# Kernel tuning notes

Measured on AMD Instinct MI355X. Metric: run time of the kernel, lower is better.

Reference implementation:

```python
import jax, jax.numpy as jnp
import numpy as np

B, T, N, DIN = 32, 12, 512, 1
H, K, ED, HOR, OD = 64, 3, 10, 12, 1


def setup_inputs() -> dict:
    key = jax.random.key(0)
    ks = jax.random.split(key, 15)
    rn = lambda k, s, sc=0.1: jax.random.normal(k, s, jnp.float32) * sc
    return {
        "source": jax.random.normal(ks[0], (B, T, N, DIN), jnp.float32),
        "targets": jax.random.normal(ks[1], (B, HOR, N, OD), jnp.float32),
        # standard Gumbel(0,1) noise: -log(Exp(1)), matches torch's exponential_().log()
        "gumbel_noise": -jnp.log(jax.random.exponential(ks[2], (N, N, 2), jnp.float32)),
        "emb": jax.random.normal(ks[3], (N, ED), jnp.float32),
        "gw0": rn(ks[4], (ED, K, DIN + H, 2 * H)),
        "gb0": rn(ks[5], (ED, 2 * H)),
        "uw0": rn(ks[6], (ED, K, DIN + H, H)),
        "ub0": rn(ks[7], (ED, H)),
        "gw1": rn(ks[8], (ED, K, 2 * H, 2 * H)),
        "gb1": rn(ks[9], (ED, 2 * H)),
        "uw1": rn(ks[10], (ED, K, 2 * H, H)),
        "ub1": rn(ks[11], (ED, H)),
        "cw": rn(ks[12], (HOR * OD, 1, 1, H)),  # Conv2d(1, HOR*OD, (1, H)) weight
        "cb": rn(ks[13], (HOR * OD,)),
    }


def scaled_laplacian(emb, gnoise):
    sim = emb @ emb.T                                   # [N,N]
    nrm = jnp.linalg.norm(emb, axis=1, keepdims=True)
    lg = sim / (nrm @ nrm.T)
    lg = (lg + 1.0) / 2.0
    logits = jnp.stack([lg, 1.0 - lg], axis=-1)         # [N,N,2]
    # faithful to the pasted gumbel_softmax: y_soft = gumbels (no softmax), tau=1, hard=True
    y_soft = logits + gnoise
    idx = jnp.argmax(y_soft, axis=-1)
    y_hard = jax.nn.one_hot(idx, 2, dtype=logits.dtype)
    ret = y_hard - jax.lax.stop_gradient(y_soft) + y_soft
    adj = ret[:, :, 0] * (1.0 - jnp.eye(N, dtype=logits.dtype))  # zero diagonal
    d = jnp.sum(adj, axis=1)
    L = -adj + jnp.diag(d)                              # diag(adj)=0, so L diag = d
    lam = jnp.max(L) - jnp.min(L)
    tilde = 2.0 * L / lam - jnp.eye(N, dtype=logits.dtype)
    return tilde


def cheb_supports(tilde):
    sup = [jnp.eye(N, dtype=tilde.dtype), tilde]
    for _ in range(2, K):
        sup.append(2.0 * tilde @ sup[-1] - sup[-2])
    return jnp.stack(sup, axis=0)                       # [K,N,N]


def gconv(x, emb, supports, wp, bp):
    # x: [B,N,C]; wp: [ED,K,C,O]; bp: [ED,O]
    xg = jnp.einsum('knm,bmc->bnkc', supports, x)
    w = jnp.einsum('nd,dkio->nkio', emb, wp)
    b = emb @ bp                                        # [N,O]
    return jnp.einsum('bnki,nkio->bno', xg, w) + b


def run_layer(inputs, emb, supports, gw, gb, uw, ub):
    # inputs: [B,T,N,C] -> hidden states [B,T,N,H]
    h0 = jnp.zeros((inputs.shape[0], N, H), inputs.dtype)

    def step(h, x_t):
        xs = jnp.concatenate([x_t, h], axis=-1)
        zr = jax.nn.sigmoid(gconv(xs, emb, supports, gw, gb))
        z, r = zr[..., :H], zr[..., H:]
        cand = jnp.concatenate([x_t, z * h], axis=-1)
        hc = jnp.tanh(gconv(cand, emb, supports, uw, ub))
        h_new = r * h + (1.0 - r) * hc
        return h_new, h_new

    _, hs = jax.lax.scan(step, h0, jnp.swapaxes(inputs, 0, 1))
    return jnp.swapaxes(hs, 0, 1)


def reference(source, targets, gumbel_noise, emb, gw0, gb0, uw0, ub0,
              gw1, gb1, uw1, ub1, cw, cb):
    tilde = scaled_laplacian(emb, gumbel_noise)
    supports = cheb_supports(tilde)
    h1 = run_layer(source, emb, supports, gw0, gb0, uw0, ub0)
    h2 = run_layer(h1, emb, supports, gw1, gb1, uw1, ub1)
    last = h2[:, -1, :, :]                              # [B,N,H]
    # Conv2d(1, HOR*OD, (1,H)) over [B,1,N,H] == per-node linear
    y = jnp.einsum('bnh,oh->bon', last, cw[:, 0, 0, :]) + cb[None, :, None]
    y = y.reshape(-1, HOR, OD, N)
    return jnp.transpose(y, (0, 1, 3, 2))               # [B,HOR,N,OD]
```

## Files before the change

kernel.cpp:

```cpp
#include <hip/hip_runtime.h>
#include <math.h>

#define N_    512
#define B_    32
#define T_    12
#define H_    64
#define ED_   10
#define HOR_  12
#define OUTS_ 4096

typedef unsigned short ushort_t;
typedef __attribute__((ext_vector_type(4))) float f32x4;
typedef __attribute__((ext_vector_type(8))) __bf16 bf16x8;
typedef __attribute__((ext_vector_type(8))) short short8;

__device__ __forceinline__ float sigmoidf_(float x){ return 1.f/(1.f+expf(-x)); }
__device__ __forceinline__ float b2f(ushort_t u){ return __uint_as_float(((unsigned)u)<<16); }
__device__ __forceinline__ ushort_t f2b(float f){
  unsigned x = __float_as_uint(f);
  unsigned r = x + 0x7FFFu + ((x>>16)&1u);
  return (ushort_t)(r>>16);
}
__device__ __forceinline__ void stage16(const void* g, void* l){
  __builtin_amdgcn_global_load_lds(
    (const __attribute__((address_space(1))) unsigned int*)g,
    (__attribute__((address_space(3))) unsigned int*)l, 16, 0, 0);
}

__global__ __launch_bounds__(512) void k_norm(const float* __restrict__ emb, float* __restrict__ nrm){
  int n = threadIdx.x;
  if (n < N_){
    float s = 0.f;
    #pragma unroll
    for (int d=0; d<ED_; ++d){ float v = emb[n*ED_+d]; s += v*v; }
    nrm[n] = sqrtf(s);
  }
}

__global__ __launch_bounds__(256) void k_adj(const float* __restrict__ emb, const float* __restrict__ nrm,
                      const float* __restrict__ gn, ushort_t* __restrict__ Abf, float* __restrict__ dvec){
  __shared__ float ei[ED_];
  __shared__ float red[256];
  int i = blockIdx.x;
  if (threadIdx.x < ED_) ei[threadIdx.x] = emb[i*ED_+threadIdx.x];
  __syncthreads();
  float ni = nrm[i];
  float part = 0.f;
  for (int j = threadIdx.x; j < N_; j += 256){
    float dot = 0.f;
    #pragma unroll
    for (int d=0; d<ED_; ++d) dot += ei[d]*emb[j*ED_+d];
    float lg = (dot/(ni*nrm[j]) + 1.f)*0.5f;
    size_t gi = ((size_t)i*N_ + j)*2;
    float y0 = lg + gn[gi];
    float y1 = (1.f - lg) + gn[gi+1];
    bool a = (j != i && y0 >= y1);
    Abf[(size_t)i*N_ + j] = a ? (ushort_t)0x3F80 : (ushort_t)0;
    part += a ? 1.f : 0.f;
  }
  red[threadIdx.x] = part;
  __syncthreads();
  for (int s=128; s>0; s>>=1){
    if (threadIdx.x < s) red[threadIdx.x] += red[threadIdx.x+s];
    __syncthreads();
  }
  if (threadIdx.x==0) dvec[i] = red[0];
}

__global__ __launch_bounds__(512) void k_lam(const float* __restrict__ dvec, float* __restrict__ lam){
  __shared__ float red[512];
  red[threadIdx.x] = dvec[threadIdx.x];
  __syncthreads();
  for (int s=256; s>0; s>>=1){
    if (threadIdx.x < s) red[threadIdx.x] = fmaxf(red[threadIdx.x], red[threadIdx.x+s]);
    __syncthreads();
  }
  if (threadIdx.x==0){
    float maxd = red[0];
    lam[0] = maxd + (maxd > 0.f ? 1.f : 0.f);
  }
}

__global__ __launch_bounds__(256) void k_a2(const ushort_t* __restrict__ Abf, ushort_t* __restrict__ A2bf){
  __shared__ float ar[N_];
  int n = blockIdx.x;
  for (int p = threadIdx.x; p < N_; p += 256) ar[p] = b2f(Abf[(size_t)n*N_ + p]);
  __syncthreads();
  int m0 = threadIdx.x, m1 = threadIdx.x + 256;
  float a0 = 0.f, a1 = 0.f;
  for (int p=0; p<N_; ++p){
    float ap = ar[p];
    a0 += ap * b2f(Abf[(size_t)p*N_ + m0]);
    a1 += ap * b2f(Abf[(size_t)p*N_ + m1]);
  }
  A2bf[(size_t)n*N_ + m0] = f2b(a0);
  A2bf[(size_t)n*N_ + m1] = f2b(a1);
}

__global__ __launch_bounds__(256) void k_admats(const ushort_t* __restrict__ Abf, const float* __restrict__ dvec,
                        const float* __restrict__ lam, ushort_t* __restrict__ ADh){
  int idx = blockIdx.x*256 + threadIdx.x;
  int m = idx & (N_-1);
  float dm = 2.f*dvec[m]/lam[0] - 1.f;
  ADh[idx] = Abf[idx] ? f2b(dm) : (ushort_t)0;
}

__global__ __launch_bounds__(256) void k_apply(
    const ushort_t* __restrict__ XH, const ushort_t* __restrict__ XL,
    const ushort_t* __restrict__ Abf, const ushort_t* __restrict__ A2bf, const ushort_t* __restrict__ ADh,
    float* __restrict__ P, float* __restrict__ Rm, float* __restrict__ Qm)
{
  __shared__ ushort_t lds[5*4096];
  const int cBase = blockIdx.x<<6, nBase = blockIdx.y<<6;
  const int tid = threadIdx.x, lane = tid&63, w = tid>>6;
  const int lrow = lane>>3, lslot = lane&7;
  const int srck = lslot ^ (lrow&7);
  f32x4 acc[3][4];
  #pragma unroll
  for (int i=0;i<3;++i)
    #pragma unroll
    for (int j=0;j<4;++j) acc[i][j] = f32x4{0.f,0.f,0.f,0.f};
  const int fl = lane&15, kq = lane>>4;

  for (int kk=0; kk<512; kk+=64){
    #pragma unroll
    for (int s=0; s<10; ++s){
      int instId = w + s*4;
      int tile = instId>>3;
      int inst = instId&7;
      const char* g = (tile==0)? (const char*)XH : (tile==1)? (const char*)XL :
                      (tile==2)? (const char*)Abf : (tile==3)? (const char*)A2bf : (const char*)ADh;
      int rb = (tile<2? cBase : nBase) + inst*8 + lrow;
      stage16(g + (size_t)rb*(N_*2) + kk*2 + srck*16,
              (char*)lds + tile*8192 + inst*1024);
    }
    __syncthreads();
    #pragma unroll
    for (int kh=0; kh<2; ++kh){
      int rowA = (w<<4) + fl;
      int offA = (rowA<<6) + (((kq + (kh<<2)) ^ (rowA&7))<<3);
      bf16x8 ah  = *(const bf16x8*)&lds[offA];
      bf16x8 alo = *(const bf16x8*)&lds[4096 + offA];
      bf16x8 bA[4], b2[4], bD[4];
      #pragma unroll
      for (int fj=0; fj<4; ++fj){
        int rowB = (fj<<4) + fl;
        int offB = (rowB<<6) + (((kq + (kh<<2)) ^ (rowB&7))<<3);
        bA[fj] = *(const bf16x8*)&lds[2*4096 + offB];
        b2[fj] = *(const bf16x8*)&lds[3*4096 + offB];
        bD[fj] = *(const bf16x8*)&lds[4*4096 + offB];
      }
      #pragma unroll
      for (int fj=0; fj<4; ++fj){
        acc[0][fj] = __builtin_amdgcn_mfma_f32_16x16x32_bf16(ah,  bA[fj], acc[0][fj], 0,0,0);
        acc[0][fj] = __builtin_amdgcn_mfma_f32_16x16x32_bf16(alo, bA[fj], acc[0][fj], 0,0,0);
        acc[1][fj] = __builtin_amdgcn_mfma_f32_16x16x32_bf16(ah,  b2[fj], acc[1][fj], 0,0,0);
        acc[1][fj] = __builtin_amdgcn_mfma_f32_16x16x32_bf16(alo, b2[fj], acc[1][fj], 0,0,0);
        acc[2][fj] = __builtin_amdgcn_mfma_f32_16x16x32_bf16(ah,  bD[fj], acc[2][fj], 0,0,0);
        acc[2][fj] = __builtin_amdgcn_mfma_f32_16x16x32_bf16(alo, bD[fj], acc[2][fj], 0,0,0);
      }
    }
    __syncthreads();
  }
  int cg = cBase + (w<<4) + (kq<<2);
  #pragma unroll
  for (int fj=0; fj<4; ++fj){
    int ng = nBase + (fj<<4) + fl;
    *(float4*)&P [(size_t)ng*OUTS_ + cg] = make_float4(acc[0][fj][0],acc[0][fj][1],acc[0][fj][2],acc[0][fj][3]);
    *(float4*)&Rm[(size_t)ng*OUTS_ + cg] = make_float4(acc[1][fj][0],acc[1][fj][1],acc[1][fj][2],acc[1][fj][3]);
    *(float4*)&Qm[(size_t)ng*OUTS_ + cg] = make_float4(acc[2][fj][0],acc[2][fj][1],acc[2][fj][2],acc[2][fj][3]);
  }
}

__global__ __launch_bounds__(256) void k_wmax(const float* __restrict__ wp, const float* __restrict__ emb,
                       float* __restrict__ scratch, int KIO, int O){
  __shared__ float es[N_*ED_];
  __shared__ float sm[256];
  for (int e = threadIdx.x; e < N_*ED_; e += 256) es[e] = emb[e];
  __syncthreads();
  int e = blockIdx.x*256 + threadIdx.x;
  float m = 0.f;
  if (e < KIO){
    float wv[ED_];
    #pragma unroll
    for (int d=0; d<ED_; ++d) wv[d] = wp[(size_t)d*KIO + e];
    int n0 = blockIdx.y*256;
    for (int n=n0; n<n0+256; ++n){
      float a = 0.f;
      #pragma unroll
      for (int d=0; d<ED_; ++d) a += es[n*ED_+d]*wv[d];
      m = fmaxf(m, fabsf(a));
    }
  }
  sm[threadIdx.x] = m;
  __syncthreads();
  for (int s=128; s>=O; s>>=1){
    if (threadIdx.x < s) sm[threadIdx.x] = fmaxf(sm[threadIdx.x], sm[threadIdx.x+s]);
    __syncthreads();
  }
  if (threadIdx.x < O)
    scratch[(size_t)(blockIdx.x*gridDim.y + blockIdx.y)*O + threadIdx.x] = sm[threadIdx.x];
}

__global__ __launch_bounds__(256) void k_wred(const float* __restrict__ scratch,
                       float* __restrict__ sb, int nb, int O){
  __shared__ float sm[256];
  int o = blockIdx.x;
  float m = 0.f;
  for (int b = threadIdx.x; b < nb; b += 256)
    m = fmaxf(m, scratch[(size_t)b*O + o]);
  sm[threadIdx.x] = m;
  __syncthreads();
  for (int s=128; s>0; s>>=1){
    if (threadIdx.x < s) sm[threadIdx.x] = fmaxf(sm[threadIdx.x], sm[threadIdx.x+s]);
    __syncthreads();
  }
  if (threadIdx.x==0) sb[o] = sm[0];
}

__global__ __launch_bounds__(256) void k_wquant(const float* __restrict__ wp, const float* __restrict__ emb,
                         const float* __restrict__ sb, short* __restrict__ W,
                         int KI, int O, int RS){
  __shared__ float es[N_*ED_];
  for (int e = threadIdx.x; e < N_*ED_; e += 256) es[e] = emb[e];
  __syncthreads();
  int KC = RS/8;
  int e = blockIdx.x*256 + threadIdx.x;
  if (e >= KC*O) return;
  int o = e % O, kc = e / O;
  int KIO = KI*O;
  float M = sb[o];
  float inv = (M > 0.f) ? 32767.f/M : 0.f;
  float wv[8][ED_];
  #pragma unroll
  for (int km=0; km<8; ++km){
    int ki = kc*8 + km;
    #pragma unroll
    for (int d=0; d<ED_; ++d)
      wv[km][d] = (ki < KI) ? wp[(size_t)d*KIO + (size_t)ki*O + o] : 0.f;
  }
  int n0 = blockIdx.y*32;
  for (int n=n0; n<n0+32; ++n){
    short8 q;
    #pragma unroll
    for (int km=0; km<8; ++km){
      float a = 0.f;
      #pragma unroll
      for (int d=0; d<ED_; ++d) a += es[n*ED_+d]*wv[km][d];
      q[km] = (short)__float2int_rn(a*inv);
    }
    *(short8*)&W[(((size_t)n*KC + kc)*O + o)*8] = q;
  }
}

__global__ __launch_bounds__(256) void k_bias(const float* __restrict__ bp, const float* __restrict__ emb,
                       float* __restrict__ Bo, int O){
  int idx = blockIdx.x*256 + threadIdx.x;
  int o = idx % O, n = idx / O;
  float a = 0.f;
  #pragma unroll
  for (int d=0; d<ED_; ++d) a += emb[n*ED_+d]*bp[d*O+o];
  Bo[idx] = a;
}

__global__ void k_fill0(float* __restrict__ p, size_t n){
  size_t i = (size_t)blockIdx.x*blockDim.x + threadIdx.x;
  size_t stride = (size_t)gridDim.x*blockDim.x;
  for (; i<n; i+=stride) p[i] = 0.f;
}

__global__ __launch_bounds__(256) void k_btr(const float* __restrict__ S0, const float* __restrict__ S1,
        ushort_t* __restrict__ XH, ushort_t* __restrict__ XL, int CIN, int coff0, int coff1,
        const float* __restrict__ src, int t, int doSrc){
  __shared__ float Tt[64][65];
  const float* S = blockIdx.z ? S1 : S0;
  int coff = blockIdx.z ? coff1 : coff0;
  int mt = blockIdx.x, b = blockIdx.y;
  int r = threadIdx.x >> 6;
  int j = threadIdx.x & 63;
  #pragma unroll
  for (int rr=0; rr<16; ++rr){
    int m = mt*64 + rr*4 + r;
    Tt[rr*4+r][j] = S[((size_t)m*B_ + b)*H_ + j];
  }
  if (doSrc && blockIdx.z==0 && threadIdx.x < 64){
    int m = mt*64 + threadIdx.x;
    float x = src[((size_t)(b*T_+t))*N_ + m];
    size_t o = ((size_t)(b*CIN))*N_ + m;
    ushort_t xh = f2b(x);
    XH[o] = xh; XL[o] = f2b(x - b2f(xh));
  }
  __syncthreads();
  int mr = threadIdx.x & 63;
  int jq = threadIdx.x >> 6;
  #pragma unroll
  for (int jj=0; jj<16; ++jj){
    int jcol = jj*4 + jq;
    float x = Tt[mr][jcol];
    size_t idx = ((size_t)(b*CIN + coff + jcol))*N_ + mt*64 + mr;
    ushort_t xh = f2b(x);
    XH[idx] = xh;
    XL[idx] = f2b(x - b2f(xh));
  }
}

template<int KC, int NBJ, int OSTR, int AS>
__device__ __forceinline__ void contract_i16(const short* __restrict__ Wb,
                                             const float* __restrict__ A0,
                                             float acc[4][NBJ]){
  short8 w0,w1,w2,w3, p0,p1,p2,p3, q0,q1,q2,q3;
  {
    const short8* wp8 = (const short8*)(Wb);
    w0=wp8[0]; w1=wp8[1]; w2=wp8[2]; w3=wp8[3];
    const short8* pp8 = (const short8*)(Wb + OSTR);
    p0=pp8[0]; p1=pp8[1]; p2=pp8[2]; p3=pp8[3];
    q0=p0; q1=p1; q2=p2; q3=p3;
  }
  for (int kc=0; kc<KC; ++kc){
    if (kc+2 < KC){
      const short8* np8 = (const short8*)(Wb + (size_t)(kc+2)*OSTR);
      q0=np8[0]; q1=np8[1]; q2=np8[2]; q3=np8[3];
    }
    #pragma unroll
    for (int kh=0; kh<2; ++kh){
      f32x4 av[NBJ];
      #pragma unroll
      for (int bj=0; bj<NBJ; ++bj) av[bj] = *(const f32x4*)&A0[bj*AS + kc*8 + kh*4];
      #pragma unroll
      for (int u=0; u<4; ++u){
        float f0=(float)w0[kh*4+u], f1=(float)w1[kh*4+u];
        float f2v=(float)w2[kh*4+u], f3=(float)w3[kh*4+u];
        #pragma unroll
        for (int bj=0; bj<NBJ; ++bj){
          acc[0][bj] += av[bj][u]*f0;
          acc[1][bj] += av[bj][u]*f1;
          acc[2][bj] += av[bj][u]*f2v;
          acc[3][bj] += av[bj][u]*f3;
        }
      }
    }
    w0=p0; w1=p1; w2=p2; w3=p3;
    p0=q0; p1=q1; p2=q2; p3=q3;
  }
}

template<int CIN>
__global__ __launch_bounds__(256) void k_gate(
    const float* __restrict__ src, int t,
    const float* __restrict__ hx, const float* __restrict__ hy,
    const float* __restrict__ P, const float* __restrict__ Rm, const float* __restrict__ Qm,
    const float* __restrict__ dvec, const float* __restrict__ lam,
    const short* __restrict__ W, const float* __restrict__ Wsc, const float* __restrict__ Bb,
    const float* __restrict__ hstate,
    float* __restrict__ cand, float* __restrict__ rbuf)
{
  constexpr int O  = 128;
  constexpr int RS = (3*CIN + 7) & ~7;
  constexpr int KC = RS/8;
  constexpr int AS = RS + 4;
  __shared__ float A[B_*AS];
  int n = blockIdx.x;
  float lm = lam[0];
  float al = -2.f/lm;
  float dn = 2.f*dvec[n]/lm - 1.f;
  float c_r = 2.f*al*al, c_q = 2.f*al, c_p = 2.f*al*dn, c_x = 2.f*dn*dn - 1.f;
  for (int e = threadIdx.x; e < B_*CIN; e += 256){
    int b = e/CIN, c = e%CIN;
    float x;
    if (CIN==65) x = (c==0) ? src[((size_t)(b*T_+t))*N_ + n] : hx[(size_t)n*(B_*H_) + b*H_ + (c-1)];
    else         x = (c<H_) ? hx[(size_t)n*(B_*H_) + b*H_ + c] : hy[(size_t)n*(B_*H_) + b*H_ + (c-H_)];
    size_t pi = (size_t)n*OUTS_ + e;
    float pe = P[pi], re = Rm[pi], qe = Qm[pi];
    float* Ab = A + b*AS;
    Ab[c]         = x;
    Ab[CIN+c]     = al*pe + dn*x;
    Ab[2*CIN+c]   = c_r*re + c_q*qe + c_p*pe + c_x*x;
  }
  for (int e = threadIdx.x; e < B_*(AS-3*CIN); e += 256){
    int b = e/(AS-3*CIN), c = e%(AS-3*CIN);
    A[b*AS + 3*CIN + c] = 0.f;
  }
  __syncthreads();
  int ow = threadIdx.x & 31;
  int bq = threadIdx.x >> 5;
  int o0 = ow*4;
  float acc[4][4] = {};
  const short* Wb = W + ((size_t)n*KC*O + o0)*8;
  const float* A0 = A + (bq*4)*AS;
  contract_i16<KC,4,O*8,AS>(Wb, A0, acc);
  #pragma unroll
  for (int oj=0; oj<4; ++oj){
    int o = o0 + oj;
    float sc = Wsc[o]*(1.f/32767.f);
    float bias = Bb[n*O+o];
    if (o < H_){
      #pragma unroll
      for (int bj=0; bj<4; ++bj){
        int b = bq*4 + bj;
        float z = sigmoidf_(acc[oj][bj]*sc + bias);
        size_t hi = (size_t)n*(B_*H_) + b*H_ + o;
        cand[hi] = z*hstate[hi];
      }
    } else {
      int oo = o - H_;
      #pragma unroll
      for (int bj=0; bj<4; ++bj){
        int b = bq*4 + bj;
        rbuf[(size_t)n*(B_*H_) + b*H_ + oo] = sigmoidf_(acc[oj][bj]*sc + bias);
      }
    }
  }
}

template<int CIN>
__global__ __launch_bounds__(256) void k_update(
    const float* __restrict__ src, int t,
    const float* __restrict__ hx, const float* __restrict__ cand,
    const float* __restrict__ P, const float* __restrict__ Rm, const float* __restrict__ Qm,
    const float* __restrict__ dvec, const float* __restrict__ lam,
    const short* __restrict__ W, const float* __restrict__ Wsc, const float* __restrict__ Bb,
    const float* __restrict__ rbuf, float* __restrict__ h)
{
  constexpr int O  = 64;
  constexpr int RS = (3*CIN + 7) & ~7;
  constexpr int KC = RS/8;
  constexpr int AS = RS + 4;
  __shared__ float A[B_*AS];
  int n = blockIdx.x;
  float lm = lam[0];
  float al = -2.f/lm;
  float dn = 2.f*dvec[n]/lm - 1.f;
  float c_r = 2.f*al*al, c_q = 2.f*al, c_p = 2.f*al*dn, c_x = 2.f*dn*dn - 1.f;
  for (int e = threadIdx.x; e < B_*CIN; e += 256){
    int b = e/CIN, c = e%CIN;
    float x;
    if (CIN==65) x = (c==0) ? src[((size_t)(b*T_+t))*N_ + n] : cand[(size_t)n*(B_*H_) + b*H_ + (c-1)];
    else         x = (c<H_) ? hx[(size_t)n*(B_*H_) + b*H_ + c] : cand[(size_t)n*(B_*H_) + b*H_ + (c-H_)];
    size_t pi = (size_t)n*OUTS_ + e;
    float pe = P[pi], re = Rm[pi], qe = Qm[pi];
    float* Ab = A + b*AS;
    Ab[c]         = x;
    Ab[CIN+c]     = al*pe + dn*x;
    Ab[2*CIN+c]   = c_r*re + c_q*qe + c_p*pe + c_x*x;
  }
  for (int e = threadIdx.x; e < B_*(AS-3*CIN); e += 256){
    int b = e/(AS-3*CIN), c = e%(AS-3*CIN);
    A[b*AS + 3*CIN + c] = 0.f;
  }
  __syncthreads();
  int ow = threadIdx.x & 15;
  int bq = threadIdx.x >> 4;
  int o0 = ow*4;
  float acc[4][2] = {};
  const short* Wb = W + ((size_t)n*KC*O + o0)*8;
  const float* A0 = A + (bq*2)*AS;
  contract_i16<KC,2,O*8,AS>(Wb, A0, acc);
  #pragma unroll
  for (int oj=0; oj<4; ++oj){
    int o = o0 + oj;
    float sc = Wsc[o]*(1.f/32767.f);
    float bias = Bb[n*O+o];
    #pragma unroll
    for (int bj=0; bj<2; ++bj){
      int b = bq*2 + bj;
      float hc = tanhf(acc[oj][bj]*sc + bias);
      size_t hidx = (size_t)n*(B_*H_) + b*H_ + o;
      float r = rbuf[hidx];
      h[hidx] = r*h[hidx] + (1.f-r)*hc;
    }
  }
}

__global__ __launch_bounds__(256) void k_readout(const float* __restrict__ hB, const float* __restrict__ cw,
                          const float* __restrict__ cb, float* __restrict__ out){
  int idx = blockIdx.x*256 + threadIdx.x;
  int n = idx & (N_-1);
  int bo = idx >> 9;
  int o = bo % HOR_, b = bo / HOR_;
  float a = cb[o];
  #pragma unroll
  for (int j=0;j<H_;++j) a += hB[(size_t)n*(B_*H_) + b*H_ + j]*cw[o*H_+j];
  out[idx] = a;
}

extern "C" void kernel_launch(void* const* d_in, const int* in_sizes, int n_in,
                              void* d_out, int out_size, void* d_ws, size_t ws_size,
                              hipStream_t stream){
  (void)in_sizes; (void)n_in; (void)out_size; (void)ws_size;
  const float* src  = (const float*)d_in[0];
  const float* gn   = (const float*)d_in[2];
  const float* emb  = (const float*)d_in[3];
  const float* gw0  = (const float*)d_in[4];
  const float* gb0  = (const float*)d_in[5];
  const float* uw0  = (const float*)d_in[6];
  const float* ub0  = (const float*)d_in[7];
  const float* gw1  = (const float*)d_in[8];
  const float* gb1  = (const float*)d_in[9];
  const float* uw1  = (const float*)d_in[10];
  const float* ub1  = (const float*)d_in[11];
  const float* cw   = (const float*)d_in[12];
  const float* cb   = (const float*)d_in[13];
  float* out = (float*)d_out;

  const int RS0 = 200;
  const int RS1 = 384;

  char* ws = (char*)d_ws;
  size_t off = 0;
  auto alloc = [&](size_t bytes)->char*{
    char* p = ws + off; off = (off + bytes + 255) & ~(size_t)255; return p;
  };
  short* Wg0 = (short*)alloc((size_t)N_*128*RS0*2);
  short* Wu0 = (short*)alloc((size_t)N_*64*RS0*2);
  short* Wg1 = (short*)alloc((size_t)N_*128*RS1*2);
  short* Wu1 = (short*)alloc((size_t)N_*64*RS1*2);
  float* Sg0 = (float*)alloc(128*4);
  float* Su0 = (float*)alloc(64*4);
  float* Sg1 = (float*)alloc(128*4);
  float* Su1 = (float*)alloc(64*4);
  float* wscr = (float*)alloc((size_t)512*128*4);
  float* Bg0 = (float*)alloc((size_t)N_*128*4);
  float* Bu0 = (float*)alloc((size_t)N_*64*4);
  float* Bg1 = (float*)alloc((size_t)N_*128*4);
  float* Bu1 = (float*)alloc((size_t)N_*64*4);
  ushort_t* Abf  = (ushort_t*)alloc((size_t)N_*N_*2);
  ushort_t* A2bf = (ushort_t*)alloc((size_t)N_*N_*2);
  ushort_t* ADh  = (ushort_t*)alloc((size_t)N_*N_*2);
  float* dvec = (float*)alloc(N_*4);
  float* lam  = (float*)alloc(256);
  float* nrm  = (float*)alloc(N_*4);
  float* hA   = (float*)alloc((size_t)N_*B_*H_*4);
  float* hB   = (float*)alloc((size_t)N_*B_*H_*4);
  float* rbuf = (float*)alloc((size_t)N_*B_*H_*4);
  float* cand = (float*)alloc((size_t)N_*B_*H_*4);
  ushort_t* XH = (ushort_t*)alloc((size_t)4096*N_*2);
  ushort_t* XL = (ushort_t*)alloc((size_t)4096*N_*2);
  float* P  = (float*)alloc((size_t)N_*OUTS_*4);
  float* R  = (float*)alloc((size_t)N_*OUTS_*4);
  float* Q  = (float*)alloc((size_t)N_*OUTS_*4);

  k_norm<<<1,512,0,stream>>>(emb, nrm);
  k_adj<<<N_,256,0,stream>>>(emb, nrm, gn, Abf, dvec);
  k_lam<<<1,512,0,stream>>>(dvec, lam);
  k_a2<<<N_,256,0,stream>>>(Abf, A2bf);
  k_admats<<<(N_*N_)/256,256,0,stream>>>(Abf, dvec, lam, ADh);

  k_wmax<<<dim3(98,2),256,0,stream>>>(gw0, emb, wscr, 195*128, 128);
  k_wred<<<128,256,0,stream>>>(wscr, Sg0, 196, 128);
  k_wmax<<<dim3(49,2),256,0,stream>>>(uw0, emb, wscr, 195*64, 64);
  k_wred<<<64,256,0,stream>>>(wscr, Su0, 98, 64);
  k_wmax<<<dim3(192,2),256,0,stream>>>(gw1, emb, wscr, 384*128, 128);
  k_wred<<<128,256,0,stream>>>(wscr, Sg1, 384, 128);
  k_wmax<<<dim3(96,2),256,0,stream>>>(uw1, emb, wscr, 384*64, 64);
  k_wred<<<64,256,0,stream>>>(wscr, Su1, 192, 64);
  k_wquant<<<dim3((25*128+255)/256,16),256,0,stream>>>(gw0, emb, Sg0, Wg0, 195, 128, RS0);
  k_wquant<<<dim3((25*64+255)/256,16),256,0,stream>>>(uw0, emb, Su0, Wu0, 195, 64, RS0);
  k_wquant<<<dim3((48*128)/256,16),256,0,stream>>>(gw1, emb, Sg1, Wg1, 384, 128, RS1);
  k_wquant<<<dim3((48*64)/256,16),256,0,stream>>>(uw1, emb, Su1, Wu1, 384, 64, RS1);
  k_bias<<<(N_*128)/256,256,0,stream>>>(gb0, emb, Bg0, 128);
  k_bias<<<(N_*64)/256,256,0,stream>>>(ub0, emb, Bu0, 64);
  k_bias<<<(N_*128)/256,256,0,stream>>>(gb1, emb, Bg1, 128);
  k_bias<<<(N_*64)/256,256,0,stream>>>(ub1, emb, Bu1, 64);

  k_fill0<<<2048,256,0,stream>>>(hA, (size_t)N_*B_*H_);
  k_fill0<<<2048,256,0,stream>>>(hB, (size_t)N_*B_*H_);

  for (int t=0; t<T_; ++t){
    k_btr<<<dim3(8,32,1),256,0,stream>>>(hA, hA, XH, XL, 65, 1, 1, src, t, 1);
    k_apply<<<dim3(34,8),256,0,stream>>>(XH, XL, Abf, A2bf, ADh, P, R, Q);
    k_gate<65><<<N_,256,0,stream>>>(src, t, hA, hA, P, R, Q, dvec, lam,
                                    Wg0, Sg0, Bg0, hA, cand, rbuf);
    k_btr<<<dim3(8,32,1),256,0,stream>>>(cand, cand, XH, XL, 65, 1, 1, nullptr, 0, 0);
    k_apply<<<dim3(34,8),256,0,stream>>>(XH, XL, Abf, A2bf, ADh, P, R, Q);
    k_update<65><<<N_,256,0,stream>>>(src, t, hA, cand, P, R, Q, dvec, lam,
                                      Wu0, Su0, Bu0, rbuf, hA);
    k_btr<<<dim3(8,32,2),256,0,stream>>>(hA, hB, XH, XL, 128, 0, 64, nullptr, 0, 0);
    k_apply<<<dim3(64,8),256,0,stream>>>(XH, XL, Abf, A2bf, ADh, P, R, Q);
    k_gate<128><<<N_,256,0,stream>>>(nullptr, 0, hA, hB, P, R, Q, dvec, lam,
                                     Wg1, Sg1, Bg1, hB, cand, rbuf);
    k_btr<<<dim3(8,32,1),256,0,stream>>>(cand, cand, XH, XL, 128, 64, 64, nullptr, 0, 0);
    k_apply<<<dim3(64,8),256,0,stream>>>(XH, XL, Abf, A2bf, ADh, P, R, Q);
    k_update<128><<<N_,256,0,stream>>>(nullptr, 0, hA, cand, P, R, Q, dvec, lam,
                                       Wu1, Su1, Bu1, rbuf, hB);
  }

  k_readout<<<(B_*HOR_*N_)/256,256,0,stream>>>(hB, cw, cb, out);
}
```

Measured before the change: 2.696 ms.

## Split layer-1 gate and update contractions over K into two blocks per node

Layer-1 gate and update graph-conv contractions now run as a split-K pair of blocks per node. Each block stages half of the 384-long reduction into shared memory and writes partial sums to a workspace buffer. A separate combine kernel adds the partials and applies the sigmoid or tanh epilogue with the GRU state update. This doubles the number of blocks and halves the per-block shared-memory staging, aiming for better occupancy. The cost is extra launches and a round trip of partial sums through global memory. It falls back to the old path if the workspace is too small.

Measured after the change: 3.139 ms. 1.16x slower.

```diff
diff --git a/kernel.cpp b/kernel.cpp
--- a/kernel.cpp
+++ b/kernel.cpp
@@ -471,6 +471,152 @@
   }
 }
 
+__global__ __launch_bounds__(256) void k_gate2(
+    const float* __restrict__ hx, const float* __restrict__ hy,
+    const float* __restrict__ P, const float* __restrict__ Rm, const float* __restrict__ Qm,
+    const float* __restrict__ dvec, const float* __restrict__ lam,
+    const short* __restrict__ W, float* __restrict__ pbuf)
+{
+  const int O = 128, KC = 48, KCH = 24, ASH = 196;
+  __shared__ float A[B_*ASH];
+  int n = blockIdx.x, y = blockIdx.y;
+  float lm = lam[0];
+  float al = -2.f/lm;
+  float dn = 2.f*dvec[n]/lm - 1.f;
+  float c_r = 2.f*al*al, c_q = 2.f*al, c_p = 2.f*al*dn, c_x = 2.f*dn*dn - 1.f;
+  for (int e = threadIdx.x; e < B_*192; e += 256){
+    int b = e/192, kl = e%192;
+    int ki = y*192 + kl;
+    int s = ki >> 7, c = ki & 127;
+    float x = (c<H_) ? hx[(size_t)n*(B_*H_) + b*H_ + c] : hy[(size_t)n*(B_*H_) + b*H_ + (c-H_)];
+    float v;
+    if (s==0) v = x;
+    else {
+      size_t pi = (size_t)n*OUTS_ + b*128 + c;
+      float pe = P[pi];
+      if (s==1) v = al*pe + dn*x;
+      else { float re = Rm[pi], qe = Qm[pi]; v = c_r*re + c_q*qe + c_p*pe + c_x*x; }
+    }
+    A[b*ASH + kl] = v;
+  }
+  __syncthreads();
+  int ow = threadIdx.x & 31;
+  int bq = threadIdx.x >> 5;
+  int o0 = ow*4;
+  float acc[4][4] = {};
+  const short* Wb = W + ((size_t)n*KC*O + o0)*8 + (size_t)y*KCH*O*8;
+  const float* A0 = A + (bq*4)*ASH;
+  contract_i16<KCH,4,O*8,ASH>(Wb, A0, acc);
+  float* pb = pbuf + (((size_t)y*N_ + n)*256 + threadIdx.x)*16;
+  #pragma unroll
+  for (int oj=0; oj<4; ++oj)
+    *(float4*)&pb[oj*4] = make_float4(acc[oj][0], acc[oj][1], acc[oj][2], acc[oj][3]);
+}
+
+__global__ __launch_bounds__(256) void k_combg(const float* __restrict__ pbuf,
+    const float* __restrict__ Wsc, const float* __restrict__ Bb, const float* __restrict__ hstate,
+    float* __restrict__ cand, float* __restrict__ rbuf)
+{
+  int n = blockIdx.x, tid = threadIdx.x;
+  const float* p0 = pbuf + ((size_t)n*256 + tid)*16;
+  const float* p1 = pbuf + (((size_t)N_ + n)*256 + tid)*16;
+  int ow = tid & 31, bq = tid >> 5, o0 = ow*4;
+  #pragma unroll
+  for (int oj=0; oj<4; ++oj){
+    float4 u = *(const float4*)&p0[oj*4];
+    float4 v = *(const float4*)&p1[oj*4];
+    float av[4] = {u.x+v.x, u.y+v.y, u.z+v.z, u.w+v.w};
+    int o = o0 + oj;
+    float sc = Wsc[o]*(1.f/32767.f);
+    float bias = Bb[n*128 + o];
+    if (o < H_){
+      #pragma unroll
+      for (int bj=0; bj<4; ++bj){
+        int b = bq*4 + bj;
+        float z = sigmoidf_(av[bj]*sc + bias);
+        size_t hi = (size_t)n*(B_*H_) + b*H_ + o;
+        cand[hi] = z*hstate[hi];
+      }
+    } else {
+      int oo = o - H_;
+      #pragma unroll
+      for (int bj=0; bj<4; ++bj){
+        int b = bq*4 + bj;
+        rbuf[(size_t)n*(B_*H_) + b*H_ + oo] = sigmoidf_(av[bj]*sc + bias);
+      }
+    }
+  }
+}
+
+__global__ __launch_bounds__(256) void k_upd2(
+    const float* __restrict__ hx, const float* __restrict__ cand,
+    const float* __restrict__ P, const float* __restrict__ Rm, const float* __restrict__ Qm,
+    const float* __restrict__ dvec, const float* __restrict__ lam,
+    const short* __restrict__ W, float* __restrict__ pbuf)
+{
+  const int O = 64, KC = 48, KCH = 24, ASH = 196;
+  __shared__ float A[B_*ASH];
+  int n = blockIdx.x, y = blockIdx.y;
+  float lm = lam[0];
+  float al = -2.f/lm;
+  float dn = 2.f*dvec[n]/lm - 1.f;
+  float c_r = 2.f*al*al, c_q = 2.f*al, c_p = 2.f*al*dn, c_x = 2.f*dn*dn - 1.f;
+  for (int e = threadIdx.x; e < B_*192; e += 256){
+    int b = e/192, kl = e%192;
+    int ki = y*192 + kl;
+    int s = ki >> 7, c = ki & 127;
+    float x = (c<H_) ? hx[(size_t)n*(B_*H_) + b*H_ + c] : cand[(size_t)n*(B_*H_) + b*H_ + (c-H_)];
+    float v;
+    if (s==0) v = x;
+    else {
+      size_t pi = (size_t)n*OUTS_ + b*128 + c;
+      float pe = P[pi];
+      if (s==1) v = al*pe + dn*x;
+      else { float re = Rm[pi], qe = Qm[pi]; v = c_r*re + c_q*qe + c_p*pe + c_x*x; }
+    }
+    A[b*ASH + kl] = v;
+  }
+  __syncthreads();
+  int ow = threadIdx.x & 15;
+  int bq = threadIdx.x >> 4;
+  int o0 = ow*4;
+  float acc[4][2] = {};
+  const short* Wb = W + ((size_t)n*KC*O + o0)*8 + (size_t)y*KCH*O*8;
+  const float* A0 = A + (bq*2)*ASH;
+  contract_i16<KCH,2,O*8,ASH>(Wb, A0, acc);
+  float* pb = pbuf + (((size_t)y*N_ + n)*256 + threadIdx.x)*8;
+  #pragma unroll
+  for (int oj=0; oj<4; ++oj){
+    pb[oj*2]   = acc[oj][0];
+    pb[oj*2+1] = acc[oj][1];
+  }
+}
+
+__global__ __launch_bounds__(256) void k_combu(const float* __restrict__ pbuf,
+    const float* __restrict__ Wsc, const float* __restrict__ Bb,
+    const float* __restrict__ rbuf, float* __restrict__ h)
+{
+  int n = blockIdx.x, tid = threadIdx.x;
+  const float* p0 = pbuf + ((size_t)n*256 + tid)*8;
+  const float* p1 = pbuf + (((size_t)N_ + n)*256 + tid)*8;
+  int ow = tid & 15, bq = tid >> 4, o0 = ow*4;
+  #pragma unroll
+  for (int oj=0; oj<4; ++oj){
+    int o = o0 + oj;
+    float sc = Wsc[o]*(1.f/32767.f);
+    float bias = Bb[n*64 + o];
+    #pragma unroll
+    for (int bj=0; bj<2; ++bj){
+      int b = bq*2 + bj;
+      float a = p0[oj*2+bj] + p1[oj*2+bj];
+      float hc = tanhf(a*sc + bias);
+      size_t hidx = (size_t)n*(B_*H_) + b*H_ + o;
+      float r = rbuf[hidx];
+      h[hidx] = r*h[hidx] + (1.f-r)*hc;
+    }
+  }
+}
+
 __global__ __launch_bounds__(256) void k_readout(const float* __restrict__ hB, const float* __restrict__ cw,
                           const float* __restrict__ cb, float* __restrict__ out){
   int idx = blockIdx.x*256 + threadIdx.x;
@@ -486,7 +632,7 @@
 extern "C" void kernel_launch(void* const* d_in, const int* in_sizes, int n_in,
                               void* d_out, int out_size, void* d_ws, size_t ws_size,
                               hipStream_t stream){
-  (void)in_sizes; (void)n_in; (void)out_size; (void)ws_size;
+  (void)in_sizes; (void)n_in; (void)out_size;
   const float* src  = (const float*)d_in[0];
   const float* gn   = (const float*)d_in[2];
   const float* emb  = (const float*)d_in[3];
@@ -538,6 +684,8 @@
   float* P  = (float*)alloc((size_t)N_*OUTS_*4);
   float* R  = (float*)alloc((size_t)N_*OUTS_*4);
   float* Q  = (float*)alloc((size_t)N_*OUTS_*4);
+  float* pbuf = (float*)alloc((size_t)2*N_*256*16*4);
+  const bool ksplit = (off <= ws_size);
 
   k_norm<<<1,512,0,stream>>>(emb, nrm);
   k_adj<<<N_,256,0,stream>>>(emb, nrm, gn, Abf, dvec);
@@ -576,12 +724,22 @@
                                       Wu0, Su0, Bu0, rbuf, hA);
     k_btr<<<dim3(8,32,2),256,0,stream>>>(hA, hB, XH, XL, 128, 0, 64, nullptr, 0, 0);
     k_apply<<<dim3(64,8),256,0,stream>>>(XH, XL, Abf, A2bf, ADh, P, R, Q);
-    k_gate<128><<<N_,256,0,stream>>>(nullptr, 0, hA, hB, P, R, Q, dvec, lam,
-                                     Wg1, Sg1, Bg1, hB, cand, rbuf);
+    if (ksplit){
+      k_gate2<<<dim3(N_,2),256,0,stream>>>(hA, hB, P, R, Q, dvec, lam, Wg1, pbuf);
+      k_combg<<<N_,256,0,stream>>>(pbuf, Sg1, Bg1, hB, cand, rbuf);
+    } else {
+      k_gate<128><<<N_,256,0,stream>>>(nullptr, 0, hA, hB, P, R, Q, dvec, lam,
+                                       Wg1, Sg1, Bg1, hB, cand, rbuf);
+    }
     k_btr<<<dim3(8,32,1),256,0,stream>>>(cand, cand, XH, XL, 128, 64, 64, nullptr, 0, 0);
     k_apply<<<dim3(64,8),256,0,stream>>>(XH, XL, Abf, A2bf, ADh, P, R, Q);
-    k_update<128><<<N_,256,0,stream>>>(nullptr, 0, hA, cand, P, R, Q, dvec, lam,
-                                       Wu1, Su1, Bu1, rbuf, hB);
+    if (ksplit){
+      k_upd2<<<dim3(N_,2),256,0,stream>>>(hA, cand, P, R, Q, dvec, lam, Wu1, pbuf);
+      k_combu<<<N_,256,0,stream>>>(pbuf, Su1, Bu1, rbuf, hB);
+    } else {
+      k_update<128><<<N_,256,0,stream>>>(nullptr, 0, hA, cand, P, R, Q, dvec, lam,
+                                         Wu1, Su1, Bu1, rbuf, hB);
+    }
   }
 
   k_readout<<<(B_*HOR_*N_)/256,256,0,stream>>>(hB, cw, cb, out);
```
